# Optimization experiments

Hardware: AMD Instinct MI355X
Metric: run time of the kernel (lower is better)

The kernel has to match this reference:

```python
import jax, jax.numpy as jnp
import numpy as np
from jax import lax

D_IN = 512      # input_size
H = 256         # hidden_size
GRU_IN = H + D_IN  # flowdelta_step prepends residual (H) to the input


def setup_inputs() -> dict:
    key = jax.random.key(0)
    kx, k1, k2, k3, k4 = jax.random.split(key, 5)
    B, T = 128, 1024
    x = jax.random.normal(kx, (B, T, D_IN), dtype=jnp.float32)
    # PyTorch GRU parameter layout: weight_ih (3H, in), weight_hh (3H, H),
    # gate order [r, z, n], init U(-1/sqrt(H), 1/sqrt(H))
    s = 1.0 / np.sqrt(H)
    w_ih = jax.random.uniform(k1, (3 * H, GRU_IN), jnp.float32, -s, s)
    w_hh = jax.random.uniform(k2, (3 * H, H), jnp.float32, -s, s)
    b_ih = jax.random.uniform(k3, (3 * H,), jnp.float32, -s, s)
    b_hh = jax.random.uniform(k4, (3 * H,), jnp.float32, -s, s)
    return {"x": x, "w_ih": w_ih, "w_hh": w_hh, "b_ih": b_ih, "b_hh": b_hh}


def reference(x, w_ih, w_hh, b_ih, b_hh):
    # x: (B, T, D). FlowRNN transposes to (T, B, D) and loops over T,
    # feeding one step at a time with carried hidden -> equivalent to a
    # single unidirectional GRU scan whose step input is [residual, x_t],
    # residual_t = h_{t-1} - h_{t-2} (zeros before t=1), logged pre-update.
    B = x.shape[0]
    xs = jnp.swapaxes(x, 0, 1)  # (T, B, D)

    def step(carry, x_t):
        h_prev, res = carry                                  # (B,H), (B,H)
        inp = jnp.concatenate([res, x_t], axis=-1)           # (B, H+D)
        gx = inp @ w_ih.T + b_ih                             # (B, 3H)
        gh = h_prev @ w_hh.T + b_hh                          # (B, 3H)
        r = jax.nn.sigmoid(gx[:, :H] + gh[:, :H])
        z = jax.nn.sigmoid(gx[:, H:2 * H] + gh[:, H:2 * H])
        n = jnp.tanh(gx[:, 2 * H:] + r * gh[:, 2 * H:])
        h_new = (1.0 - z) * n + z * h_prev
        new_res = h_new - h_prev                             # flowdelta
        return (h_new, new_res), (h_new, res)

    h0 = jnp.zeros((B, H), x.dtype)
    res0 = jnp.zeros((B, H), x.dtype)
    _, (outs, ress) = lax.scan(step, (h0, res0), xs)
    output = jnp.swapaxes(outs, 0, 1)           # (B, T, H)
    residual_output = jnp.swapaxes(ress, 0, 1)  # (B, T, H)
    return output, residual_output
```

## Files before the change

kernel.cpp:

```cpp
#include <hip/hip_runtime.h>


typedef __attribute__((ext_vector_type(8))) short bf16x8_t;
typedef __attribute__((ext_vector_type(4))) float f32x4_t;

#define MFMA16(a, b, c) __builtin_amdgcn_mfma_f32_16x16x32_bf16((a), (b), (c), 0, 0, 0)

constexpr int Bb = 128, Tt = 1024, Dd = 512, Hh = 256;
constexpr int Gg = 8;
constexpr int Ss = 8;
constexpr int ROWS = Bb / Gg;
constexpr int Wj = Hh / Ss;
constexpr unsigned FLAG_TARGET = Ss * 4;

__device__ __forceinline__ short f2bf(float f) {
  union { float f; unsigned int u; } v; v.f = f;
  unsigned int r = v.u + 0x7fffu + ((v.u >> 16) & 1u);
  return (short)(r >> 16);
}

__device__ __forceinline__ bf16x8_t load8_bf(const float* p) {
  const f32x4_t a = *(const f32x4_t*)p;
  const f32x4_t b = *(const f32x4_t*)(p + 4);
  bf16x8_t r;
  r[0] = f2bf(a[0]); r[1] = f2bf(a[1]); r[2] = f2bf(a[2]); r[3] = f2bf(a[3]);
  r[4] = f2bf(b[0]); r[5] = f2bf(b[1]); r[6] = f2bf(b[2]); r[7] = f2bf(b[3]);
  return r;
}

__device__ __forceinline__ bf16x8_t ringload(const unsigned short* p) {
  unsigned long long lo = __hip_atomic_load((const unsigned long long*)p,
                                            __ATOMIC_RELAXED, __HIP_MEMORY_SCOPE_AGENT);
  unsigned long long hi = __hip_atomic_load((const unsigned long long*)(p + 4),
                                            __ATOMIC_RELAXED, __HIP_MEMORY_SCOPE_AGENT);
  union { unsigned long long u[2]; bf16x8_t v; } r;
  r.u[0] = lo; r.u[1] = hi; return r.v;
}

__global__ __launch_bounds__(256, 1)
void flowrnn_scan(const float* __restrict__ x, const float* __restrict__ w_ih,
                  const float* __restrict__ w_hh, const float* __restrict__ b_ih,
                  const float* __restrict__ b_hh, float* __restrict__ out,
                  unsigned int* __restrict__ ws) {
  __shared__ short xstage[ROWS][520];
  __shared__ float accS[ROWS][260];
  __shared__ float hpown[ROWS][Wj];
  __shared__ float biasR[Wj], biasZ[Wj], biasNX[Wj], biasNH[Wj];

  const int tid  = threadIdx.x;
  const int wid  = tid >> 6;
  const int lane = tid & 63;
  const int n16  = lane & 15;
  const int q    = lane >> 4;
  const int g    = blockIdx.x >> 3;
  const int s    = blockIdx.x & 7;
  const int j0   = Wj * s;

  unsigned int* arrive = ws;
  unsigned short* hring = (unsigned short*)(ws + Gg * Tt);
  unsigned short* rring = hring + 2 * Bb * Hh;
  float* rout = out + (size_t)Bb * Tt * Hh;

  if (tid < Wj) {
    int j = tid;
    biasR[j]  = b_ih[j0 + j]        + b_hh[j0 + j];
    biasZ[j]  = b_ih[256 + j0 + j]  + b_hh[256 + j0 + j];
    biasNX[j] = b_ih[512 + j0 + j];
    biasNH[j] = b_hh[512 + j0 + j];
  }
  ((float*)hpown)[tid] = 0.f;
  ((float*)hpown)[tid + 256] = 0.f;

  bf16x8_t brz[16], bn[8], bxp[16], bxs[8];
  {
    int grow = (wid < 2) ? (j0 + wid * 16 + n16) : (256 + j0 + (wid - 2) * 16 + n16);
    for (int c = 0; c < 8; ++c)
      brz[c] = load8_bf(w_ih + (size_t)grow * 768 + c * 32 + q * 8);
    for (int c = 0; c < 8; ++c)
      brz[8 + c] = load8_bf(w_hh + (size_t)grow * 256 + c * 32 + q * 8);
  }
  if (wid < 2) {
    int grow = 512 + j0 + wid * 16 + n16;
    for (int c = 0; c < 8; ++c)
      bn[c] = load8_bf(w_ih + (size_t)grow * 768 + c * 32 + q * 8);
  } else {
    int grow = 512 + j0 + (wid - 2) * 16 + n16;
    for (int c = 0; c < 8; ++c)
      bn[c] = load8_bf(w_hh + (size_t)grow * 256 + c * 32 + q * 8);
  }
  {
    int tp = (wid == 3) ? 5 : wid * 2;
    int grow = (tp >> 1) * 256 + j0 + (tp & 1) * 16 + n16;
    for (int c = 0; c < 16; ++c)
      bxp[c] = load8_bf(w_ih + (size_t)grow * 768 + 256 + c * 32 + q * 8);
    int ts = (wid < 2) ? 1 : 3;
    int gs = (ts >> 1) * 256 + j0 + (ts & 1) * 16 + n16;
    int cbase = (wid & 1) ? 8 : 0;
    for (int c = 0; c < 8; ++c)
      bxs[c] = load8_bf(w_ih + (size_t)gs * 768 + 256 + (cbase + c) * 32 + q * 8);
  }

  const int xrow = tid >> 4, xseg = tid & 15;
  const float* xbase = x + (size_t)(g * ROWS + xrow) * Tt * Dd + xseg * 32;
  f32x4_t xpre[8];
  {
    const f32x4_t* xp = (const f32x4_t*)(xbase);
#pragma unroll
    for (int i = 0; i < 8; ++i) xpre[i] = xp[i];
  }
  __syncthreads();

  long spin_budget = 50000000;

  for (int t = 0; t < Tt; ++t) {
    {
      bf16x8_t* dst = (bf16x8_t*)&xstage[xrow][xseg * 32];
#pragma unroll
      for (int i = 0; i < 4; ++i) {
        f32x4_t a = xpre[2 * i], b = xpre[2 * i + 1];
        bf16x8_t v;
        v[0] = f2bf(a[0]); v[1] = f2bf(a[1]); v[2] = f2bf(a[2]); v[3] = f2bf(a[3]);
        v[4] = f2bf(b[0]); v[5] = f2bf(b[1]); v[6] = f2bf(b[2]); v[7] = f2bf(b[3]);
        dst[i] = v;
      }
    }
    __syncthreads();

    if (t + 1 < Tt) {
      const f32x4_t* xp = (const f32x4_t*)(xbase + (size_t)(t + 1) * Dd);
#pragma unroll
      for (int i = 0; i < 8; ++i) xpre[i] = xp[i];
    }

    f32x4_t accP = {0.f, 0.f, 0.f, 0.f}, accSx = {0.f, 0.f, 0.f, 0.f};
    {
      bf16x8_t xa[16];
      for (int c = 0; c < 16; ++c)
        xa[c] = *(const bf16x8_t*)&xstage[n16][c * 32 + q * 8];
      for (int c = 0; c < 16; ++c)
        accP = MFMA16(xa[c], bxp[c], accP);
      int cbase = (wid & 1) ? 8 : 0;
      for (int c = 0; c < 8; ++c)
        accSx = MFMA16(xa[cbase + c], bxs[c], accSx);
    }

    f32x4_t accRZ = {0.f, 0.f, 0.f, 0.f}, accN = {0.f, 0.f, 0.f, 0.f};
    if (t > 0) {
      const unsigned int* fp = arrive + g * Tt + (t - 1);
      for (;;) {
        unsigned int v = 0;
        if (lane == 0)
          v = __hip_atomic_load(fp, __ATOMIC_RELAXED, __HIP_MEMORY_SCOPE_AGENT);
        v = (unsigned int)__shfl((int)v, 0, 64);
        if (v >= FLAG_TARGET) break;
        __builtin_amdgcn_s_sleep(1);
        if (--spin_budget < 0) break;
      }
      const int slot = (t - 1) & 1;
      const unsigned short* hb = hring + (size_t)slot * (Bb * Hh);
      const unsigned short* rb = rring + (size_t)slot * (Bb * Hh);
      const int b = g * ROWS + n16;
      bf16x8_t rf[8], hf[8];
      for (int c = 0; c < 8; ++c) {
        rf[c] = ringload(rb + (size_t)b * Hh + c * 32 + q * 8);
        hf[c] = ringload(hb + (size_t)b * Hh + c * 32 + q * 8);
      }
      for (int c = 0; c < 8; ++c) accRZ = MFMA16(rf[c], brz[c], accRZ);
      for (int c = 0; c < 8; ++c) accRZ = MFMA16(hf[c], brz[8 + c], accRZ);
      if (wid < 2) { for (int c = 0; c < 8; ++c) accN = MFMA16(rf[c], bn[c], accN); }
      else         { for (int c = 0; c < 8; ++c) accN = MFMA16(hf[c], bn[c], accN); }
    }

    {
      const int r0 = q * 4;
      for (int i = 0; i < 4; ++i) accS[r0 + i][wid * 16 + n16] = accRZ[i];
      const int nb = (wid < 2) ? (64 + wid * 16) : (96 + (wid - 2) * 16);
      for (int i = 0; i < 4; ++i) accS[r0 + i][nb + n16] = accN[i];
      const int pc = (wid == 0) ? 128 : (wid == 1) ? 176 : (wid == 2) ? 224 : 240;
      for (int i = 0; i < 4; ++i) accS[r0 + i][pc + n16] = accP[i];
      const int sc = 144 + 16 * wid + ((wid >= 2) ? 16 : 0);
      for (int i = 0; i < 4; ++i) accS[r0 + i][sc + n16] = accSx[i];
    }
    __syncthreads();

    {
      const int row = tid >> 4;
      const int jp  = (tid & 15) * 2;
      float hnew[2], resv[2];
#pragma unroll
      for (int u = 0; u < 2; ++u) {
        const int j = jp + u;
        float ar  = accS[row][j];
        float az  = accS[row][32 + j];
        float anx = accS[row][64 + j];
        float anh = accS[row][96 + j];
        float xr = (j < 16) ? accS[row][128 + j] : (accS[row][144 + j - 16] + accS[row][160 + j - 16]);
        float xz = (j < 16) ? accS[row][176 + j] : (accS[row][192 + j - 16] + accS[row][208 + j - 16]);
        float xn = (j < 16) ? accS[row][224 + j] : accS[row][240 + j - 16];
        float rg = 1.f / (1.f + __expf(-(ar + xr + biasR[j])));
        float zg = 1.f / (1.f + __expf(-(az + xz + biasZ[j])));
        float narg = (anx + xn + biasNX[j]) + rg * (anh + biasNH[j]);
        float e2 = __expf(2.f * narg);
        float ng = 1.f - 2.f / (e2 + 1.f);
        float hp = hpown[row][j];
        float h  = (1.f - zg) * ng + zg * hp;
        hnew[u] = h; resv[u] = h - hp;
      }
      const int b = g * ROWS + row;
      const int slot = t & 1;
      unsigned int hp32 = ((unsigned int)(unsigned short)f2bf(hnew[0])) |
                          ((unsigned int)(unsigned short)f2bf(hnew[1]) << 16);
      unsigned int rp32 = ((unsigned int)(unsigned short)f2bf(resv[0])) |
                          ((unsigned int)(unsigned short)f2bf(resv[1]) << 16);
      unsigned int* hd = (unsigned int*)(hring + (size_t)slot * (Bb * Hh) + (size_t)b * Hh + j0 + jp);
      unsigned int* rd = (unsigned int*)(rring + (size_t)slot * (Bb * Hh) + (size_t)b * Hh + j0 + jp);
      __hip_atomic_store(hd, hp32, __ATOMIC_RELAXED, __HIP_MEMORY_SCOPE_AGENT);
      __hip_atomic_store(rd, rp32, __ATOMIC_RELAXED, __HIP_MEMORY_SCOPE_AGENT);
      float* op = out + ((size_t)b * Tt + t) * Hh + j0 + jp;
      op[0] = hnew[0]; op[1] = hnew[1];
      if (t == 0) {
        float* rp0 = rout + ((size_t)b * Tt) * Hh + j0 + jp;
        rp0[0] = 0.f; rp0[1] = 0.f;
      }
      if (t + 1 < Tt) {
        float* rp = rout + ((size_t)b * Tt + t + 1) * Hh + j0 + jp;
        rp[0] = resv[0]; rp[1] = resv[1];
      }
      hpown[row][jp]     = hnew[0];
      hpown[row][jp + 1] = hnew[1];
    }

    __builtin_amdgcn_s_waitcnt(0);
    if (lane == 0)
      __hip_atomic_fetch_add(arrive + g * Tt + t, 1u,
                             __ATOMIC_RELAXED, __HIP_MEMORY_SCOPE_AGENT);
  }
}

extern "C" void kernel_launch(void* const* d_in, const int* in_sizes, int n_in,
                              void* d_out, int out_size, void* d_ws, size_t ws_size,
                              hipStream_t stream) {
  const float* x    = (const float*)d_in[0];
  const float* w_ih = (const float*)d_in[1];
  const float* w_hh = (const float*)d_in[2];
  const float* b_ih = (const float*)d_in[3];
  const float* b_hh = (const float*)d_in[4];
  float* out = (float*)d_out;

  hipMemsetAsync(d_ws, 0, (size_t)Gg * Tt * sizeof(unsigned int), stream);

  flowrnn_scan<<<Gg * Ss, 256, 0, stream>>>(x, w_ih, w_hh, b_ih, b_hh, out,
                                            (unsigned int*)d_ws);
}
```

Before: 10.35 ms.

## Replace cross-block flag sync with single-workgroup-per-batch-group GRU scan

Each 16-row batch group now runs in one 1024-thread workgroup that owns all 256 hidden columns. Hidden state and residual go through double-buffered LDS instead of global rings polled with atomic flags, so the per-step inter-block spin-wait and global round trip disappear. The x tile is double-buffered in LDS to cut barriers to one per step, and the accSum shuffle through shared memory is removed because each wave holds every gate for its columns. In exchange only 8 workgroups run, each doing 8x the MFMA work per step and holding far more weight registers per thread, which risks spills and leaves most CUs idle.

Measured after the change: 38.39 ms. 3.71x slower.

```diff
diff --git a/kernel.cpp b/kernel.cpp
--- a/kernel.cpp
+++ b/kernel.cpp
@@ -7,11 +7,10 @@
 #define MFMA16(a, b, c) __builtin_amdgcn_mfma_f32_16x16x32_bf16((a), (b), (c), 0, 0, 0)
 
 constexpr int Bb = 128, Tt = 1024, Dd = 512, Hh = 256;
-constexpr int Gg = 8;
-constexpr int Ss = 8;
-constexpr int ROWS = Bb / Gg;
-constexpr int Wj = Hh / Ss;
-constexpr unsigned FLAG_TARGET = Ss * 4;
+constexpr int NB = 8;
+constexpr int ROWS = 16;
+constexpr int XST = 520;
+constexpr int HST = 264;
 
 __device__ __forceinline__ short f2bf(float f) {
   union { float f; unsigned int u; } v; v.f = f;
@@ -28,218 +27,138 @@
   return r;
 }
 
-__device__ __forceinline__ bf16x8_t ringload(const unsigned short* p) {
-  unsigned long long lo = __hip_atomic_load((const unsigned long long*)p,
-                                            __ATOMIC_RELAXED, __HIP_MEMORY_SCOPE_AGENT);
-  unsigned long long hi = __hip_atomic_load((const unsigned long long*)(p + 4),
-                                            __ATOMIC_RELAXED, __HIP_MEMORY_SCOPE_AGENT);
-  union { unsigned long long u[2]; bf16x8_t v; } r;
-  r.u[0] = lo; r.u[1] = hi; return r.v;
-}
-
-__global__ __launch_bounds__(256, 1)
+__global__ __launch_bounds__(1024, 1)
 void flowrnn_scan(const float* __restrict__ x, const float* __restrict__ w_ih,
                   const float* __restrict__ w_hh, const float* __restrict__ b_ih,
-                  const float* __restrict__ b_hh, float* __restrict__ out,
-                  unsigned int* __restrict__ ws) {
-  __shared__ short xstage[ROWS][520];
-  __shared__ float accS[ROWS][260];
-  __shared__ float hpown[ROWS][Wj];
-  __shared__ float biasR[Wj], biasZ[Wj], biasNX[Wj], biasNH[Wj];
+                  const float* __restrict__ b_hh, float* __restrict__ out) {
+  __shared__ short xs[2][ROWS][XST];
+  __shared__ short hsb[2][ROWS][HST];
+  __shared__ short rsb[2][ROWS][HST];
 
   const int tid  = threadIdx.x;
   const int wid  = tid >> 6;
   const int lane = tid & 63;
   const int n16  = lane & 15;
   const int q    = lane >> 4;
-  const int g    = blockIdx.x >> 3;
-  const int s    = blockIdx.x & 7;
-  const int j0   = Wj * s;
+  const int g    = blockIdx.x;
 
-  unsigned int* arrive = ws;
-  unsigned short* hring = (unsigned short*)(ws + Gg * Tt);
-  unsigned short* rring = hring + 2 * Bb * Hh;
   float* rout = out + (size_t)Bb * Tt * Hh;
 
-  if (tid < Wj) {
-    int j = tid;
-    biasR[j]  = b_ih[j0 + j]        + b_hh[j0 + j];
-    biasZ[j]  = b_ih[256 + j0 + j]  + b_hh[256 + j0 + j];
-    biasNX[j] = b_ih[512 + j0 + j];
-    biasNH[j] = b_hh[512 + j0 + j];
-  }
-  ((float*)hpown)[tid] = 0.f;
-  ((float*)hpown)[tid + 256] = 0.f;
-
-  bf16x8_t brz[16], bn[8], bxp[16], bxs[8];
+  bf16x8_t bx[3][16];
+  bf16x8_t br[3][8];
+  bf16x8_t bh[3][8];
   {
-    int grow = (wid < 2) ? (j0 + wid * 16 + n16) : (256 + j0 + (wid - 2) * 16 + n16);
-    for (int c = 0; c < 8; ++c)
-      brz[c] = load8_bf(w_ih + (size_t)grow * 768 + c * 32 + q * 8);
-    for (int c = 0; c < 8; ++c)
-      brz[8 + c] = load8_bf(w_hh + (size_t)grow * 256 + c * 32 + q * 8);
-  }
-  if (wid < 2) {
-    int grow = 512 + j0 + wid * 16 + n16;
-    for (int c = 0; c < 8; ++c)
-      bn[c] = load8_bf(w_ih + (size_t)grow * 768 + c * 32 + q * 8);
-  } else {
-    int grow = 512 + j0 + (wid - 2) * 16 + n16;
-    for (int c = 0; c < 8; ++c)
-      bn[c] = load8_bf(w_hh + (size_t)grow * 256 + c * 32 + q * 8);
-  }
-  {
-    int tp = (wid == 3) ? 5 : wid * 2;
-    int grow = (tp >> 1) * 256 + j0 + (tp & 1) * 16 + n16;
-    for (int c = 0; c < 16; ++c)
-      bxp[c] = load8_bf(w_ih + (size_t)grow * 768 + 256 + c * 32 + q * 8);
-    int ts = (wid < 2) ? 1 : 3;
-    int gs = (ts >> 1) * 256 + j0 + (ts & 1) * 16 + n16;
-    int cbase = (wid & 1) ? 8 : 0;
-    for (int c = 0; c < 8; ++c)
-      bxs[c] = load8_bf(w_ih + (size_t)gs * 768 + 256 + (cbase + c) * 32 + q * 8);
+    const int gr0 = 16 * wid + n16;
+#pragma unroll
+    for (int gi = 0; gi < 3; ++gi) {
+      const int grow = gi * 256 + gr0;
+      const float* wi = w_ih + (size_t)grow * 768;
+      const float* wh = w_hh + (size_t)grow * 256;
+#pragma unroll
+      for (int c = 0; c < 16; ++c) bx[gi][c] = load8_bf(wi + 256 + c * 32 + q * 8);
+#pragma unroll
+      for (int c = 0; c < 8; ++c)  br[gi][c] = load8_bf(wi + c * 32 + q * 8);
+#pragma unroll
+      for (int c = 0; c < 8; ++c)  bh[gi][c] = load8_bf(wh + c * 32 + q * 8);
+    }
   }
 
-  const int xrow = tid >> 4, xseg = tid & 15;
-  const float* xbase = x + (size_t)(g * ROWS + xrow) * Tt * Dd + xseg * 32;
-  f32x4_t xpre[8];
+  const int j = 16 * wid + n16;
+  const float bR  = b_ih[j] + b_hh[j];
+  const float bZ  = b_ih[256 + j] + b_hh[256 + j];
+  const float bNX = b_ih[512 + j];
+  const float bNH = b_hh[512 + j];
+
+  for (int i = tid; i < ROWS * HST; i += 1024) {
+    ((short*)hsb[0])[i] = 0;
+    ((short*)rsb[0])[i] = 0;
+  }
+
+  const int xrow = tid >> 6;
+  const int xcol = (tid & 63) * 8;
+  const float* xbase = x + ((size_t)(g * ROWS + xrow) * Tt) * Dd + xcol;
+  f32x4_t xpa = *(const f32x4_t*)xbase;
+  f32x4_t xpb = *(const f32x4_t*)(xbase + 4);
   {
-    const f32x4_t* xp = (const f32x4_t*)(xbase);
-#pragma unroll
-    for (int i = 0; i < 8; ++i) xpre[i] = xp[i];
+    bf16x8_t v;
+    v[0] = f2bf(xpa[0]); v[1] = f2bf(xpa[1]); v[2] = f2bf(xpa[2]); v[3] = f2bf(xpa[3]);
+    v[4] = f2bf(xpb[0]); v[5] = f2bf(xpb[1]); v[6] = f2bf(xpb[2]); v[7] = f2bf(xpb[3]);
+    *(bf16x8_t*)&xs[0][xrow][xcol] = v;
   }
+
+  float hprev[4] = {0.f, 0.f, 0.f, 0.f};
   __syncthreads();
 
-  long spin_budget = 50000000;
-
   for (int t = 0; t < Tt; ++t) {
-    {
-      bf16x8_t* dst = (bf16x8_t*)&xstage[xrow][xseg * 32];
-#pragma unroll
-      for (int i = 0; i < 4; ++i) {
-        f32x4_t a = xpre[2 * i], b = xpre[2 * i + 1];
-        bf16x8_t v;
-        v[0] = f2bf(a[0]); v[1] = f2bf(a[1]); v[2] = f2bf(a[2]); v[3] = f2bf(a[3]);
-        v[4] = f2bf(b[0]); v[5] = f2bf(b[1]); v[6] = f2bf(b[2]); v[7] = f2bf(b[3]);
-        dst[i] = v;
-      }
-    }
-    __syncthreads();
+    const int cur = t & 1, nxt = (t + 1) & 1;
 
     if (t + 1 < Tt) {
       const f32x4_t* xp = (const f32x4_t*)(xbase + (size_t)(t + 1) * Dd);
-#pragma unroll
-      for (int i = 0; i < 8; ++i) xpre[i] = xp[i];
+      xpa = xp[0]; xpb = xp[1];
     }
 
-    f32x4_t accP = {0.f, 0.f, 0.f, 0.f}, accSx = {0.f, 0.f, 0.f, 0.f};
-    {
-      bf16x8_t xa[16];
-      for (int c = 0; c < 16; ++c)
-        xa[c] = *(const bf16x8_t*)&xstage[n16][c * 32 + q * 8];
-      for (int c = 0; c < 16; ++c)
-        accP = MFMA16(xa[c], bxp[c], accP);
-      int cbase = (wid & 1) ? 8 : 0;
-      for (int c = 0; c < 8; ++c)
-        accSx = MFMA16(xa[cbase + c], bxs[c], accSx);
+    f32x4_t aR  = {0.f, 0.f, 0.f, 0.f};
+    f32x4_t aZ  = {0.f, 0.f, 0.f, 0.f};
+    f32x4_t aNX = {0.f, 0.f, 0.f, 0.f};
+    f32x4_t aNH = {0.f, 0.f, 0.f, 0.f};
+#pragma unroll
+    for (int c = 0; c < 16; ++c) {
+      bf16x8_t f = *(const bf16x8_t*)&xs[cur][n16][c * 32 + q * 8];
+      aR  = MFMA16(f, bx[0][c], aR);
+      aZ  = MFMA16(f, bx[1][c], aZ);
+      aNX = MFMA16(f, bx[2][c], aNX);
+    }
+#pragma unroll
+    for (int c = 0; c < 8; ++c) {
+      bf16x8_t f = *(const bf16x8_t*)&rsb[cur][n16][c * 32 + q * 8];
+      aR  = MFMA16(f, br[0][c], aR);
+      aZ  = MFMA16(f, br[1][c], aZ);
+      aNX = MFMA16(f, br[2][c], aNX);
+    }
+#pragma unroll
+    for (int c = 0; c < 8; ++c) {
+      bf16x8_t f = *(const bf16x8_t*)&hsb[cur][n16][c * 32 + q * 8];
+      aR  = MFMA16(f, bh[0][c], aR);
+      aZ  = MFMA16(f, bh[1][c], aZ);
+      aNH = MFMA16(f, bh[2][c], aNH);
     }
 
-    f32x4_t accRZ = {0.f, 0.f, 0.f, 0.f}, accN = {0.f, 0.f, 0.f, 0.f};
-    if (t > 0) {
-      const unsigned int* fp = arrive + g * Tt + (t - 1);
-      for (;;) {
-        unsigned int v = 0;
-        if (lane == 0)
-          v = __hip_atomic_load(fp, __ATOMIC_RELAXED, __HIP_MEMORY_SCOPE_AGENT);
-        v = (unsigned int)__shfl((int)v, 0, 64);
-        if (v >= FLAG_TARGET) break;
-        __builtin_amdgcn_s_sleep(1);
-        if (--spin_budget < 0) break;
-      }
-      const int slot = (t - 1) & 1;
-      const unsigned short* hb = hring + (size_t)slot * (Bb * Hh);
-      const unsigned short* rb = rring + (size_t)slot * (Bb * Hh);
-      const int b = g * ROWS + n16;
-      bf16x8_t rf[8], hf[8];
-      for (int c = 0; c < 8; ++c) {
-        rf[c] = ringload(rb + (size_t)b * Hh + c * 32 + q * 8);
-        hf[c] = ringload(hb + (size_t)b * Hh + c * 32 + q * 8);
-      }
-      for (int c = 0; c < 8; ++c) accRZ = MFMA16(rf[c], brz[c], accRZ);
-      for (int c = 0; c < 8; ++c) accRZ = MFMA16(hf[c], brz[8 + c], accRZ);
-      if (wid < 2) { for (int c = 0; c < 8; ++c) accN = MFMA16(rf[c], bn[c], accN); }
-      else         { for (int c = 0; c < 8; ++c) accN = MFMA16(hf[c], bn[c], accN); }
+    if (t + 1 < Tt) {
+      bf16x8_t v;
+      v[0] = f2bf(xpa[0]); v[1] = f2bf(xpa[1]); v[2] = f2bf(xpa[2]); v[3] = f2bf(xpa[3]);
+      v[4] = f2bf(xpb[0]); v[5] = f2bf(xpb[1]); v[6] = f2bf(xpb[2]); v[7] = f2bf(xpb[3]);
+      *(bf16x8_t*)&xs[nxt][xrow][xcol] = v;
     }
 
-    {
-      const int r0 = q * 4;
-      for (int i = 0; i < 4; ++i) accS[r0 + i][wid * 16 + n16] = accRZ[i];
-      const int nb = (wid < 2) ? (64 + wid * 16) : (96 + (wid - 2) * 16);
-      for (int i = 0; i < 4; ++i) accS[r0 + i][nb + n16] = accN[i];
-      const int pc = (wid == 0) ? 128 : (wid == 1) ? 176 : (wid == 2) ? 224 : 240;
-      for (int i = 0; i < 4; ++i) accS[r0 + i][pc + n16] = accP[i];
-      const int sc = 144 + 16 * wid + ((wid >= 2) ? 16 : 0);
-      for (int i = 0; i < 4; ++i) accS[r0 + i][sc + n16] = accSx[i];
-    }
-    __syncthreads();
+#pragma unroll
+    for (int i = 0; i < 4; ++i) {
+      const int row = q * 4 + i;
+      const float rg   = 1.f / (1.f + __expf(-(aR[i] + bR)));
+      const float zg   = 1.f / (1.f + __expf(-(aZ[i] + bZ)));
+      const float narg = (aNX[i] + bNX) + rg * (aNH[i] + bNH);
+      const float e2   = __expf(2.f * narg);
+      const float ng   = 1.f - 2.f / (e2 + 1.f);
+      const float h    = (1.f - zg) * ng + zg * hprev[i];
+      const float rv   = h - hprev[i];
+      hprev[i] = h;
 
-    {
-      const int row = tid >> 4;
-      const int jp  = (tid & 15) * 2;
-      float hnew[2], resv[2];
-#pragma unroll
-      for (int u = 0; u < 2; ++u) {
-        const int j = jp + u;
-        float ar  = accS[row][j];
-        float az  = accS[row][32 + j];
-        float anx = accS[row][64 + j];
-        float anh = accS[row][96 + j];
-        float xr = (j < 16) ? accS[row][128 + j] : (accS[row][144 + j - 16] + accS[row][160 + j - 16]);
-        float xz = (j < 16) ? accS[row][176 + j] : (accS[row][192 + j - 16] + accS[row][208 + j - 16]);
-        float xn = (j < 16) ? accS[row][224 + j] : accS[row][240 + j - 16];
-        float rg = 1.f / (1.f + __expf(-(ar + xr + biasR[j])));
-        float zg = 1.f / (1.f + __expf(-(az + xz + biasZ[j])));
-        float narg = (anx + xn + biasNX[j]) + rg * (anh + biasNH[j]);
-        float e2 = __expf(2.f * narg);
-        float ng = 1.f - 2.f / (e2 + 1.f);
-        float hp = hpown[row][j];
-        float h  = (1.f - zg) * ng + zg * hp;
-        hnew[u] = h; resv[u] = h - hp;
-      }
-      const int b = g * ROWS + row;
-      const int slot = t & 1;
-      unsigned int hp32 = ((unsigned int)(unsigned short)f2bf(hnew[0])) |
-                          ((unsigned int)(unsigned short)f2bf(hnew[1]) << 16);
-      unsigned int rp32 = ((unsigned int)(unsigned short)f2bf(resv[0])) |
-                          ((unsigned int)(unsigned short)f2bf(resv[1]) << 16);
-      unsigned int* hd = (unsigned int*)(hring + (size_t)slot * (Bb * Hh) + (size_t)b * Hh + j0 + jp);
-      unsigned int* rd = (unsigned int*)(rring + (size_t)slot * (Bb * Hh) + (size_t)b * Hh + j0 + jp);
-      __hip_atomic_store(hd, hp32, __ATOMIC_RELAXED, __HIP_MEMORY_SCOPE_AGENT);
-      __hip_atomic_store(rd, rp32, __ATOMIC_RELAXED, __HIP_MEMORY_SCOPE_AGENT);
-      float* op = out + ((size_t)b * Tt + t) * Hh + j0 + jp;
-      op[0] = hnew[0]; op[1] = hnew[1];
-      if (t == 0) {
-        float* rp0 = rout + ((size_t)b * Tt) * Hh + j0 + jp;
-        rp0[0] = 0.f; rp0[1] = 0.f;
-      }
-      if (t + 1 < Tt) {
-        float* rp = rout + ((size_t)b * Tt + t + 1) * Hh + j0 + jp;
-        rp[0] = resv[0]; rp[1] = resv[1];
-      }
-      hpown[row][jp]     = hnew[0];
-      hpown[row][jp + 1] = hnew[1];
+      const size_t b = (size_t)(g * ROWS + row);
+      out[(b * Tt + t) * Hh + j] = h;
+      if (t == 0)      rout[(b * Tt) * Hh + j] = 0.f;
+      if (t + 1 < Tt)  rout[(b * Tt + t + 1) * Hh + j] = rv;
+
+      hsb[nxt][row][j] = f2bf(h);
+      rsb[nxt][row][j] = f2bf(rv);
     }
 
-    __builtin_amdgcn_s_waitcnt(0);
-    if (lane == 0)
-      __hip_atomic_fetch_add(arrive + g * Tt + t, 1u,
-                             __ATOMIC_RELAXED, __HIP_MEMORY_SCOPE_AGENT);
+    __syncthreads();
   }
 }
 
 extern "C" void kernel_launch(void* const* d_in, const int* in_sizes, int n_in,
                               void* d_out, int out_size, void* d_ws, size_t ws_size,
                               hipStream_t stream) {
+  (void)in_sizes; (void)n_in; (void)out_size; (void)d_ws; (void)ws_size;
   const float* x    = (const float*)d_in[0];
   const float* w_ih = (const float*)d_in[1];
   const float* w_hh = (const float*)d_in[2];
@@ -247,8 +166,5 @@
   const float* b_hh = (const float*)d_in[4];
   float* out = (float*)d_out;
 
-  hipMemsetAsync(d_ws, 0, (size_t)Gg * Tt * sizeof(unsigned int), stream);
-
-  flowrnn_scan<<<Gg * Ss, 256, 0, stream>>>(x, w_ih, w_hh, b_ih, b_hh, out,
-                                            (unsigned int*)d_ws);
+  flowrnn_scan<<<NB, 1024, 0, stream>>>(x, w_ih, w_hh, b_ih, b_hh, out);
 }
```
